# Kernel optimization log

Hardware: AMD Instinct MI355X
Metric: run time of the kernel (lower is better)

The kernel has to match this reference:

```python
import jax, jax.numpy as jnp
import numpy as np

H = 256        # hidden_size
HEADS = 8      # conv1 heads
B = 256        # number of graphs (sessions)
L = 64         # nodes per graph (max_length)
N = B * L      # total nodes
E = 131072     # edges before self-loops
NNODE = 37000  # item vocabulary / num classes


def setup_inputs() -> dict:
    key = jax.random.key(0)
    ks = jax.random.split(key, 16)
    s = 0.02
    return {
        "x_ids": jax.random.randint(ks[0], (N,), 0, NNODE + 1),
        "edge_index": jax.random.randint(ks[1], (2, E), 0, N),
        "batch": jnp.repeat(jnp.arange(B, dtype=jnp.int32), L),
        "emb": jax.random.normal(ks[2], (NNODE + 1, H)) * s,
        "W1": jax.random.normal(ks[3], (H, HEADS * H)) * s,
        "att_src1": jax.random.normal(ks[4], (HEADS, H)) * s,
        "att_dst1": jax.random.normal(ks[5], (HEADS, H)) * s,
        "b1": jnp.zeros((HEADS * H,)),
        "W2": jax.random.normal(ks[6], (HEADS * H, H)) * s,
        "att_src2": jax.random.normal(ks[7], (1, H)) * s,
        "att_dst2": jax.random.normal(ks[8], (1, H)) * s,
        "b2": jnp.zeros((H,)),
        "Wih": jax.random.normal(ks[9], (4 * H, H)) * s,
        "Whh": jax.random.normal(ks[10], (4 * H, H)) * s,
        "bih": jnp.zeros((4 * H,)),
        "bhh": jnp.zeros((4 * H,)),
        "Wp": jax.random.normal(ks[11], (NNODE, H)) * s,
        "bp": jnp.zeros((NNODE,)),
    }


def gat_conv(x, src, dst, W, a_src, a_dst, bias, concat):
    # PyG GATConv: linear -> per-head attention logits -> leaky_relu ->
    # segment-softmax over incoming edges per dst node -> scatter-add.
    n = x.shape[0]
    heads = a_src.shape[0]
    h = (x @ W).reshape(n, heads, -1)                       # [N, heads, out]
    alpha_s = (h * a_src).sum(-1)                            # [N, heads]
    alpha_d = (h * a_dst).sum(-1)
    e = jax.nn.leaky_relu(alpha_s[src] + alpha_d[dst], 0.2)  # [E, heads]
    m = jax.ops.segment_max(e, dst, num_segments=n)
    p = jnp.exp(e - m[dst])
    z = jax.ops.segment_sum(p, dst, num_segments=n)
    alpha = p / (z[dst] + 1e-16)                             # edge softmax
    out = jax.ops.segment_sum(alpha[:, :, None] * h[src], dst, num_segments=n)
    out = out.reshape(n, -1) if concat else out.mean(axis=1)
    return out + bias


def reference(x_ids, edge_index, batch, emb, W1, att_src1, att_dst1, b1,
              W2, att_src2, att_dst2, b2, Wih, Whh, bih, bhh, Wp, bp):
    n = x_ids.shape[0]
    # GATConv default add_self_loops=True
    loops = jnp.arange(n)
    src = jnp.concatenate([edge_index[0], loops])
    dst = jnp.concatenate([edge_index[1], loops])

    emb = emb.at[0].set(0.0)  # padding_idx=0
    x = emb[x_ids]
    # eval mode: dropout is identity
    x = jax.nn.elu(gat_conv(x, src, dst, W1, att_src1, att_dst1, b1, True))
    x = gat_conv(x, src, dst, W2, att_src2, att_dst2, b2, False)  # [N, H]

    # pack variable-length graphs into padded [B, L, H] sequences
    lengths = jax.ops.segment_sum(jnp.ones((n,), jnp.int32), batch, num_segments=B)
    starts = jnp.cumsum(lengths) - lengths
    pos = jnp.arange(n) - starts[batch]
    seq = jnp.zeros((B, L, x.shape[-1]), x.dtype).at[batch, pos].set(x)
    mask = jnp.arange(L)[None, :] < lengths[:, None]  # [B, L]

    # single-layer LSTM; masking emulates pack_padded_sequence: h_n is the
    # hidden state at each sequence's true last timestep
    def step(carry, xs):
        h_prev, c_prev = carry
        x_t, m_t = xs
        g = x_t @ Wih.T + h_prev @ Whh.T + bih + bhh
        i, f, gg, o = jnp.split(g, 4, axis=-1)
        c_new = jax.nn.sigmoid(f) * c_prev + jax.nn.sigmoid(i) * jnp.tanh(gg)
        h_new = jax.nn.sigmoid(o) * jnp.tanh(c_new)
        mm = m_t[:, None]
        return (jnp.where(mm, h_new, h_prev), jnp.where(mm, c_new, c_prev)), None

    h0 = jnp.zeros((B, x.shape[-1]), x.dtype)
    (hT, _), _ = jax.lax.scan(step, (h0, h0),
                              (seq.transpose(1, 0, 2), mask.T))
    return hT @ Wp.T + bp  # [B, NNODE] scores
```

## Files before the change

### kernel.cpp

```cpp
#include <hip/hip_runtime.h>
#include <hip/hip_bf16.h>
#include <cstdint>

#define HD 256
#define NHEADS 8
#define NB 256
#define SL 64
#define NN 16384
#define NE 131072
#define NTOT (NE + NN)

typedef float floatx4 __attribute__((ext_vector_type(4)));
typedef short shortx8 __attribute__((ext_vector_type(8)));
typedef unsigned short ushortx8 __attribute__((ext_vector_type(8)));
typedef unsigned short ushortx4 __attribute__((ext_vector_type(4)));

__device__ __forceinline__ unsigned short f2bf(float f) {
    union { float f; unsigned u; } a; a.f = f;
    unsigned r = a.u + 0x7fffu + ((a.u >> 16) & 1u);
    return (unsigned short)(r >> 16);
}
__device__ __forceinline__ float bf2f(unsigned short b) {
    union { unsigned u; float f; } a; a.u = ((unsigned)b) << 16;
    return a.f;
}

__device__ __forceinline__ void store_b16_sys(unsigned short* p, unsigned v) {
    asm volatile("global_store_short %0, %1, off sc0 sc1" :: "v"(p), "v"(v) : "memory");
}
__device__ __forceinline__ shortx8 load_b128_sys(const unsigned short* p) {
    shortx8 r;
    asm volatile("global_load_dwordx4 %0, %1, off sc0 sc1" : "=v"(r) : "v"(p) : "memory");
    return r;
}


__global__ void k_cast_bf16(const float* __restrict__ in, unsigned short* __restrict__ out, int n4) {
    int i = blockIdx.x * 256 + threadIdx.x;
    if (i >= n4) return;
    float4 v = ((const float4*)in)[i];
    ushortx4 o;
    o[0] = f2bf(v.x); o[1] = f2bf(v.y); o[2] = f2bf(v.z); o[3] = f2bf(v.w);
    *(ushortx4*)&out[i * 4] = o;
}

__global__ void k_transpose_bf16(const float* __restrict__ in, unsigned short* __restrict__ out,
                                 int K, int N) {
    __shared__ float t[32][33];
    int nb = blockIdx.x * 32, kb = blockIdx.y * 32;
    int tx = threadIdx.x, ty = threadIdx.y;
#pragma unroll
    for (int i = 0; i < 4; ++i) {
        int k = kb + ty + i * 8;
        t[ty + i * 8][tx] = in[(size_t)k * N + nb + tx];
    }
    __syncthreads();
#pragma unroll
    for (int i = 0; i < 4; ++i) {
        int nrow = nb + ty + i * 8;
        out[(size_t)nrow * K + kb + tx] = f2bf(t[tx][ty + i * 8]);
    }
}

__global__ void k_add2(const float* __restrict__ a, const float* __restrict__ b,
                       float* __restrict__ o, int n) {
    int i = blockIdx.x * 256 + threadIdx.x;
    if (i < n) o[i] = a[i] + b[i];
}

__global__ void k_zero(int* __restrict__ p, int n) {
    int i = blockIdx.x * 256 + threadIdx.x;
    if (i < n) p[i] = 0;
}

__global__ void k_gather_x(const int* __restrict__ ids, const float* __restrict__ emb,
                           unsigned short* __restrict__ xb) {
    int i = blockIdx.x * 256 + threadIdx.x;
    int n = i >> 6, d4 = (i & 63) << 2;
    int id = ids[n];
    float4 v = make_float4(0.f, 0.f, 0.f, 0.f);
    if (id != 0) v = *(const float4*)&emb[(size_t)id * HD + d4];
    ushortx4 o;
    o[0] = f2bf(v.x); o[1] = f2bf(v.y); o[2] = f2bf(v.z); o[3] = f2bf(v.w);
    *(ushortx4*)&xb[(size_t)n * HD + d4] = o;
}


template <bool OUT_BF16, bool HAS_BIAS>
__global__ __launch_bounds__(256, 2) void k_gemm_bt(
    const unsigned short* __restrict__ A, const unsigned short* __restrict__ B,
    void* __restrict__ C, const float* __restrict__ bias, int M, int Nn, int K) {
    constexpr int LDT = 56;
    __shared__ unsigned short As[128 * LDT];
    __shared__ unsigned short Bs[128 * LDT];
    int tid = threadIdx.x;
    int wave = tid >> 6, lane = tid & 63;
    int q = lane >> 4, c16 = lane & 15;
    long m0 = (long)blockIdx.x * 128;
    long n0 = (long)blockIdx.y * 128;
    int wm = (wave & 1) << 6, wn = (wave >> 1) << 6;
    floatx4 acc[4][4] = {};
    int lrow = tid >> 2;
    int lk = (tid & 3) << 3;
    const unsigned short* Arow0 = A + (m0 + lrow) * K + lk;
    const unsigned short* Arow1 = A + (m0 + 64 + lrow) * K + lk;
    long nb0 = n0 + lrow;      if (nb0 >= Nn) nb0 = Nn - 1;
    long nb1 = n0 + 64 + lrow; if (nb1 >= Nn) nb1 = Nn - 1;
    const unsigned short* Brow0 = B + nb0 * K + lk;
    const unsigned short* Brow1 = B + nb1 * K + lk;

    for (int k0 = 0; k0 < K; k0 += 32) {
        ushortx8 a0 = *(const ushortx8*)(Arow0 + k0);
        ushortx8 a1 = *(const ushortx8*)(Arow1 + k0);
        ushortx8 b0 = *(const ushortx8*)(Brow0 + k0);
        ushortx8 b1 = *(const ushortx8*)(Brow1 + k0);
        __syncthreads();
        *(ushortx8*)&As[lrow * LDT + lk] = a0;
        *(ushortx8*)&As[(64 + lrow) * LDT + lk] = a1;
        *(ushortx8*)&Bs[lrow * LDT + lk] = b0;
        *(ushortx8*)&Bs[(64 + lrow) * LDT + lk] = b1;
        __syncthreads();
        shortx8 af[4], bfr[4];
#pragma unroll
        for (int mt = 0; mt < 4; ++mt)
            af[mt] = *(const shortx8*)&As[(wm + mt * 16 + c16) * LDT + q * 8];
#pragma unroll
        for (int nt = 0; nt < 4; ++nt)
            bfr[nt] = *(const shortx8*)&Bs[(wn + nt * 16 + c16) * LDT + q * 8];
#pragma unroll
        for (int mt = 0; mt < 4; ++mt)
#pragma unroll
            for (int nt = 0; nt < 4; ++nt)
                acc[mt][nt] = __builtin_amdgcn_mfma_f32_16x16x32_bf16(af[mt], bfr[nt], acc[mt][nt], 0, 0, 0);
    }
#pragma unroll
    for (int mt = 0; mt < 4; ++mt) {
        long row_base = m0 + wm + mt * 16 + q * 4;
#pragma unroll
        for (int nt = 0; nt < 4; ++nt) {
            long col = n0 + wn + nt * 16 + c16;
            if (col >= Nn) continue;
            float bv = HAS_BIAS ? bias[col] : 0.0f;
#pragma unroll
            for (int r = 0; r < 4; ++r) {
                float v = acc[mt][nt][r] + bv;
                long idx = (row_base + r) * (long)Nn + col;
                if (OUT_BF16) ((unsigned short*)C)[idx] = f2bf(v);
                else          ((float*)C)[idx] = v;
            }
        }
    }
}

__global__ __launch_bounds__(256, 2) void k_gemm_b8(
    const unsigned short* __restrict__ Ab, const unsigned short* __restrict__ W1t,
    unsigned short* __restrict__ C, const float* __restrict__ b1) {
    constexpr int LDT = 56;
    __shared__ unsigned short As[128 * LDT];
    __shared__ unsigned short Bs[128 * LDT];
    int tid = threadIdx.x;
    int wave = tid >> 6, lane = tid & 63;
    int q = lane >> 4, c16 = lane & 15;
    int hh = blockIdx.z;
    const unsigned short* A = Ab + (size_t)hh * NN * 256;
    const unsigned short* B = W1t + (size_t)hh * 256 * 256;
    long m0 = (long)blockIdx.x * 128;
    long n0 = (long)blockIdx.y * 128;
    int wm = (wave & 1) << 6, wn = (wave >> 1) << 6;
    floatx4 acc[4][4] = {};
    int lrow = tid >> 2;
    int lk = (tid & 3) << 3;
    const unsigned short* Arow0 = A + (m0 + lrow) * 256 + lk;
    const unsigned short* Arow1 = A + (m0 + 64 + lrow) * 256 + lk;
    const unsigned short* Brow0 = B + (n0 + lrow) * 256 + lk;
    const unsigned short* Brow1 = B + (n0 + 64 + lrow) * 256 + lk;

    for (int k0 = 0; k0 < 256; k0 += 32) {
        ushortx8 a0 = *(const ushortx8*)(Arow0 + k0);
        ushortx8 a1 = *(const ushortx8*)(Arow1 + k0);
        ushortx8 b0 = *(const ushortx8*)(Brow0 + k0);
        ushortx8 b1 = *(const ushortx8*)(Brow1 + k0);
        __syncthreads();
        *(ushortx8*)&As[lrow * LDT + lk] = a0;
        *(ushortx8*)&As[(64 + lrow) * LDT + lk] = a1;
        *(ushortx8*)&Bs[lrow * LDT + lk] = b0;
        *(ushortx8*)&Bs[(64 + lrow) * LDT + lk] = b1;
        __syncthreads();
        shortx8 af[4], bfr[4];
#pragma unroll
        for (int mt = 0; mt < 4; ++mt)
            af[mt] = *(const shortx8*)&As[(wm + mt * 16 + c16) * LDT + q * 8];
#pragma unroll
        for (int nt = 0; nt < 4; ++nt)
            bfr[nt] = *(const shortx8*)&Bs[(wn + nt * 16 + c16) * LDT + q * 8];
#pragma unroll
        for (int mt = 0; mt < 4; ++mt)
#pragma unroll
            for (int nt = 0; nt < 4; ++nt)
                acc[mt][nt] = __builtin_amdgcn_mfma_f32_16x16x32_bf16(af[mt], bfr[nt], acc[mt][nt], 0, 0, 0);
    }
#pragma unroll
    for (int mt = 0; mt < 4; ++mt) {
        long row_base = m0 + wm + mt * 16 + q * 4;
#pragma unroll
        for (int nt = 0; nt < 4; ++nt) {
            int gcol = hh * 256 + (int)(n0 + wn + nt * 16 + c16);
            float bv = b1[gcol];
#pragma unroll
            for (int r = 0; r < 4; ++r) {
                float v = acc[mt][nt][r] + bv;
                v = v > 0.f ? v : expm1f(v);
                C[(row_base + r) * 2048 + gcol] = f2bf(v);
            }
        }
    }
}

__global__ void k_build_v(const float* __restrict__ W1, const float* __restrict__ as1,
                          const float* __restrict__ ad1, unsigned short* __restrict__ Vb) {
    __shared__ float av[256];
    int o = blockIdx.x, k = threadIdx.x;
    int hh = o & 7;
    const float* a = (o < 8) ? as1 : ad1;
    av[k] = a[hh * 256 + k];
    __syncthreads();
    const float* wrow = W1 + (size_t)k * 2048 + hh * 256;
    float sum = 0.f;
#pragma unroll 8
    for (int d = 0; d < 256; ++d) sum += wrow[d] * av[d];
    Vb[o * 256 + k] = f2bf(sum);
}


__global__ void k_alpha2(const unsigned short* __restrict__ x2b, const float* __restrict__ asrc,
                         const float* __restrict__ adst, float* __restrict__ als,
                         float* __restrict__ ald) {
    int n = blockIdx.x, t = threadIdx.x;
    ushortx4 hv = *(const ushortx4*)&x2b[(size_t)n * 256 + t * 4];
    float s = 0.f, d = 0.f;
#pragma unroll
    for (int j = 0; j < 4; ++j) {
        float f = bf2f(hv[j]);
        s += f * asrc[t * 4 + j];
        d += f * adst[t * 4 + j];
    }
    for (int o = 32; o; o >>= 1) { s += __shfl_down(s, o, 64); d += __shfl_down(d, o, 64); }
    if (t == 0) { als[n] = s; ald[n] = d; }
}


__global__ void k_deg_init(int* __restrict__ deg) {
    int i = blockIdx.x * 256 + threadIdx.x;
    if (i < NN) deg[i] = 1;
}
__global__ void k_deg_count(const int* __restrict__ ei, int* __restrict__ deg) {
    int e = blockIdx.x * 256 + threadIdx.x;
    if (e < NE) atomicAdd(&deg[ei[NE + e]], 1);
}
__global__ void k_scan(const int* __restrict__ deg, int* __restrict__ row_start,
                       int* __restrict__ cursor) {
    __shared__ int s[1024];
    int t = threadIdx.x;
    int base = t * 16;
    int loc[16]; int sum = 0;
#pragma unroll
    for (int i = 0; i < 16; ++i) { loc[i] = deg[base + i]; sum += loc[i]; }
    s[t] = sum;
    __syncthreads();
    for (int o = 1; o < 1024; o <<= 1) {
        int v = (t >= o) ? s[t - o] : 0;
        __syncthreads();
        s[t] += v;
        __syncthreads();
    }
    int ex = s[t] - sum;
#pragma unroll
    for (int i = 0; i < 16; ++i) {
        row_start[base + i] = ex;
        cursor[base + i] = ex;
        ex += loc[i];
    }
    if (t == 0) row_start[NN] = NTOT;
}
__global__ void k_fill(const int* __restrict__ ei, int* __restrict__ cursor,
                       int* __restrict__ csr_src) {
    int e = blockIdx.x * 256 + threadIdx.x;
    if (e >= NTOT) return;
    int s, d;
    if (e < NE) { s = ei[e]; d = ei[NE + e]; }
    else        { s = e - NE; d = s; }
    int p = atomicAdd(&cursor[d], 1);
    csr_src[p] = s;
}

__global__ __launch_bounds__(256) void k_aggx(
    const int* __restrict__ row_start, const int* __restrict__ csr_src,
    const float* __restrict__ D, const unsigned short* __restrict__ xb,
    unsigned short* __restrict__ aggxb) {
    int n = blockIdx.x, t = threadIdx.x;
    int rs = row_start[n];
    int deg = row_start[n + 1] - rs;
    __shared__ float sad[8], sm[8], sinvz[8];
    __shared__ int sed[32];
    __shared__ float wlds[32][8];
    if (t < 8) sad[t] = D[n * 16 + 8 + t];
    __syncthreads();
    int hh = t >> 5, ii = t & 31;
    float adh = sad[hh];
    float lm = -1e30f;
    for (int i = ii; i < deg; i += 32) {
        int s = csr_src[rs + i];
        float e = D[s * 16 + hh] + adh;
        e = e >= 0.f ? e : 0.2f * e;
        lm = fmaxf(lm, e);
    }
    for (int o = 16; o; o >>= 1) lm = fmaxf(lm, __shfl_down(lm, o, 32));
    if (ii == 0) sm[hh] = lm;
    __syncthreads();
    float mh = sm[hh];
    float lz = 0.f;
    for (int i = ii; i < deg; i += 32) {
        int s = csr_src[rs + i];
        float e = D[s * 16 + hh] + adh;
        e = e >= 0.f ? e : 0.2f * e;
        lz += expf(e - mh);
    }
    for (int o = 16; o; o >>= 1) lz += __shfl_down(lz, o, 32);
    if (ii == 0) sinvz[hh] = 1.0f / (lz + 1e-16f);
    __syncthreads();

    float acc[8] = {0.f, 0.f, 0.f, 0.f, 0.f, 0.f, 0.f, 0.f};
    int eh = t & 7, ee = t >> 3;
    for (int base = 0; base < deg; base += 32) {
        int cnt = min(32, deg - base);
        if (t < 32) sed[t] = (t < cnt) ? csr_src[rs + base + t] : 0;
        __syncthreads();
        if (ee < cnt) {
            int s = sed[ee];
            float e = D[s * 16 + eh] + sad[eh];
            e = e >= 0.f ? e : 0.2f * e;
            wlds[ee][eh] = expf(e - sm[eh]) * sinvz[eh];
        }
        __syncthreads();
        for (int e = 0; e < cnt; ++e) {
            float xv = bf2f(xb[(size_t)sed[e] * 256 + t]);
#pragma unroll
            for (int h = 0; h < 8; ++h) acc[h] += wlds[e][h] * xv;
        }
        __syncthreads();
    }
#pragma unroll
    for (int h = 0; h < 8; ++h)
        aggxb[((size_t)h * NN + n) * 256 + t] = f2bf(acc[h]);
}


__global__ void k_agg2(const int* __restrict__ row_start, const int* __restrict__ csr_src,
                       const float* __restrict__ als, const float* __restrict__ ald,
                       const unsigned short* __restrict__ x2b, const float* __restrict__ b2,
                       unsigned short* __restrict__ out2b) {
    int n = blockIdx.x, t = threadIdx.x;
    int rs = row_start[n];
    int deg = row_start[n + 1] - rs;
    float adn = ald[n];
    float lm = -1e30f;
    for (int i = t; i < deg; i += 64) {
        float e = als[csr_src[rs + i]] + adn;
        e = e >= 0.f ? e : 0.2f * e;
        lm = fmaxf(lm, e);
    }
    for (int o = 32; o; o >>= 1) lm = fmaxf(lm, __shfl_down(lm, o, 64));
    float mh = __shfl(lm, 0, 64);
    float lz = 0.f;
    for (int i = t; i < deg; i += 64) {
        float e = als[csr_src[rs + i]] + adn;
        e = e >= 0.f ? e : 0.2f * e;
        lz += expf(e - mh);
    }
    for (int o = 32; o; o >>= 1) lz += __shfl_down(lz, o, 64);
    float zz = __shfl(lz, 0, 64);
    float inv_z = 1.0f / (zz + 1e-16f);
    float acc[4] = {0.f, 0.f, 0.f, 0.f};
    for (int i = 0; i < deg; ++i) {
        int s = csr_src[rs + i];
        float e = als[s] + adn;
        e = e >= 0.f ? e : 0.2f * e;
        float w = expf(e - mh) * inv_z;
        ushortx4 hv = *(const ushortx4*)&x2b[(size_t)s * 256 + t * 4];
#pragma unroll
        for (int j = 0; j < 4; ++j) acc[j] += w * bf2f(hv[j]);
    }
    ushortx4 o4;
#pragma unroll
    for (int j = 0; j < 4; ++j) o4[j] = f2bf(acc[j] + b2[t * 4 + j]);
    *(ushortx4*)&out2b[(size_t)n * 256 + t * 4] = o4;
}

__global__ void k_repack_whh(const unsigned short* __restrict__ Whhb,
                             unsigned short* __restrict__ WhhR) {
    int i = blockIdx.x * 256 + threadIdx.x;
    int lane = i & 63;
    int fi = i >> 6;
    int f = fi & 3, k0 = (fi >> 2) & 7, w = (fi >> 5) & 3, s = fi >> 7;
    int q = lane >> 4, c16 = lane & 15;
    int gcol = f * 256 + s * 64 + w * 16 + c16;
    int k = k0 * 32 + q * 8;
    ushortx8 v = *(const ushortx8*)&Whhb[(size_t)gcol * 256 + k];
    *(ushortx8*)&WhhR[(size_t)fi * 512 + lane * 8] = v;
}


__global__ __launch_bounds__(256, 1) void k_lstm8(
    const float* __restrict__ Xg, const unsigned short* __restrict__ WhhR,
    unsigned short* __restrict__ hX, int* __restrict__ flags) {
    __shared__ unsigned short wlds[4 * 32 * 512];

    int tid = threadIdx.x;
    int w = tid >> 6, lane = tid & 63;
    int q = lane >> 4, c16 = lane & 15;
    int g = blockIdx.x & 15, s = blockIdx.x >> 4;
    int scol = s * 64 + w * 16 + c16;
    const int fbase = g * 64;

    const unsigned short* wsrc = WhhR + (size_t)((s * 4 + w) * 32) * 512 + lane * 8;
#pragma unroll
    for (int fi = 0; fi < 32; ++fi)
        *(shortx8*)&wlds[(w * 32 + fi) * 512 + lane * 8] =
            *(const shortx8*)(wsrc + fi * 512);

    float cst[4] = {0.f, 0.f, 0.f, 0.f};

    for (int t = 0; t < SL; ++t) {
        float xg[4][4];
#pragma unroll
        for (int r = 0; r < 4; ++r) {
            const float* xp = Xg + ((size_t)(g * 16 + q * 4 + r) * SL + t) * 1024 + scol;
#pragma unroll
            for (int f = 0; f < 4; ++f) xg[r][f] = xp[f * 256];
        }

        floatx4 acc[4] = {};
        if (t > 0) {
            if (tid == 0) {
                int spins = 0;
                while (__hip_atomic_fetch_add(&flags[fbase + t - 1], 0, __ATOMIC_RELAXED,
                                              __HIP_MEMORY_SCOPE_AGENT) < 4) {
                    __builtin_amdgcn_s_sleep(2);
                    if (++spins > 65536) break;
                }
            }
            __syncthreads();

            const unsigned short* hp =
                hX + ((size_t)(t - 1) * 256 + g * 16 + c16) * 256 + q * 8;
            shortx8 af[8];
#pragma unroll
            for (int k0 = 0; k0 < 8; ++k0) af[k0] = load_b128_sys(hp + k0 * 32);
            asm volatile("s_waitcnt vmcnt(0)" ::: "memory");
            __builtin_amdgcn_sched_barrier(0);
#pragma unroll
            for (int k0 = 0; k0 < 8; ++k0)
#pragma unroll
                for (int f = 0; f < 4; ++f) {
                    shortx8 b = *(const shortx8*)&wlds[(w * 32 + k0 * 4 + f) * 512 + lane * 8];
                    acc[f] = __builtin_amdgcn_mfma_f32_16x16x32_bf16(af[k0], b, acc[f], 0, 0, 0);
                }
        }

        unsigned short* hw = hX + ((size_t)t * 256 + g * 16) * 256 + scol;
#pragma unroll
        for (int r = 0; r < 4; ++r) {
            float gi = acc[0][r] + xg[r][0];
            float gf = acc[1][r] + xg[r][1];
            float gG = acc[2][r] + xg[r][2];
            float go = acc[3][r] + xg[r][3];
            float si = __builtin_amdgcn_rcpf(1.f + __expf(-gi));
            float sf = __builtin_amdgcn_rcpf(1.f + __expf(-gf));
            float so = __builtin_amdgcn_rcpf(1.f + __expf(-go));
            float tg = 1.f - 2.f * __builtin_amdgcn_rcpf(1.f + __expf(2.f * gG));
            float c = sf * cst[r] + si * tg;
            cst[r] = c;
            float tc = 1.f - 2.f * __builtin_amdgcn_rcpf(1.f + __expf(2.f * c));
            store_b16_sys(hw + (q * 4 + r) * 256, (unsigned)f2bf(so * tc));
        }

        if (t < SL - 1) {
            asm volatile("s_waitcnt vmcnt(0)" ::: "memory");
            __syncthreads();
            if (tid == 0)
                __hip_atomic_fetch_add(&flags[fbase + t], 1, __ATOMIC_RELAXED,
                                       __HIP_MEMORY_SCOPE_AGENT);
        }
    }
}


extern "C" void kernel_launch(void* const* d_in, const int* in_sizes, int n_in,
                              void* d_out, int out_size, void* d_ws, size_t ws_size,
                              hipStream_t stream) {
    const int*   x_ids = (const int*)d_in[0];
    const int*   ei    = (const int*)d_in[1];
    const float* emb   = (const float*)d_in[3];
    const float* W1    = (const float*)d_in[4];
    const float* as1w  = (const float*)d_in[5];
    const float* ad1w  = (const float*)d_in[6];
    const float* b1    = (const float*)d_in[7];
    const float* W2    = (const float*)d_in[8];
    const float* as2w  = (const float*)d_in[9];
    const float* ad2w  = (const float*)d_in[10];
    const float* b2    = (const float*)d_in[11];
    const float* Wih   = (const float*)d_in[12];
    const float* Whh   = (const float*)d_in[13];
    const float* bih   = (const float*)d_in[14];
    const float* bhh   = (const float*)d_in[15];
    const float* Wp    = (const float*)d_in[16];
    const float* bp    = (const float*)d_in[17];

    char* ws = (char*)d_ws;
    size_t off = 0;
    auto alloc = [&](size_t bytes) -> void* {
        void* p = ws + off;
        off += (bytes + 255) & ~(size_t)255;
        return p;
    };
    unsigned short* U     = (unsigned short*)alloc((size_t)8 * NN * 256 * 2);
    unsigned short* aggxb = U;
    float*          Xg    = (float*)U;
    unsigned short* out1b = (unsigned short*)alloc((size_t)NN * 2048 * 2);
    unsigned short* hX    = out1b;
    unsigned short* xb    = (unsigned short*)alloc((size_t)NN * 256 * 2);
    unsigned short* x2b   = (unsigned short*)alloc((size_t)NN * 256 * 2);
    unsigned short* out2b = (unsigned short*)alloc((size_t)NN * 256 * 2);
    unsigned short* W1t   = (unsigned short*)alloc((size_t)2048 * 256 * 2);
    unsigned short* W2t   = (unsigned short*)alloc((size_t)256 * 2048 * 2);
    unsigned short* Wihb  = (unsigned short*)alloc((size_t)1024 * 256 * 2);
    unsigned short* Whhb  = (unsigned short*)alloc((size_t)1024 * 256 * 2);
    unsigned short* WhhR  = (unsigned short*)alloc((size_t)1024 * 256 * 2);
    unsigned short* Wpb   = (unsigned short*)alloc((size_t)37000 * 256 * 2);
    unsigned short* Vb    = (unsigned short*)alloc((size_t)16 * 256 * 2);
    float*          bb    = (float*)alloc(1024 * 4);
    float*          D     = (float*)alloc((size_t)NN * 16 * 4);
    float*          als2  = (float*)alloc((size_t)NN * 4);
    float*          ald2  = (float*)alloc((size_t)NN * 4);
    unsigned short* hTb   = (unsigned short*)alloc((size_t)256 * 256 * 2);
    int* deg       = (int*)alloc((size_t)NN * 4);
    int* row_start = (int*)alloc((size_t)(NN + 1) * 4);
    int* cursor    = (int*)alloc((size_t)NN * 4);
    int* csr_src   = (int*)alloc((size_t)NTOT * 4);
    int* flags     = (int*)alloc((size_t)16 * 64 * 4);
    (void)ws_size; (void)in_sizes; (void)n_in; (void)out_size; (void)hTb;

    k_transpose_bf16<<<dim3(2048 / 32, 256 / 32), dim3(32, 8), 0, stream>>>(W1, W1t, 256, 2048);
    k_transpose_bf16<<<dim3(256 / 32, 2048 / 32), dim3(32, 8), 0, stream>>>(W2, W2t, 2048, 256);
    k_cast_bf16<<<(262144 / 4 + 255) / 256, 256, 0, stream>>>(Wih, Wihb, 262144 / 4);
    k_cast_bf16<<<(262144 / 4 + 255) / 256, 256, 0, stream>>>(Whh, Whhb, 262144 / 4);
    k_cast_bf16<<<(9472000 / 4 + 255) / 256, 256, 0, stream>>>(Wp, Wpb, 9472000 / 4);
    k_add2<<<4, 256, 0, stream>>>(bih, bhh, bb, 1024);
    k_repack_whh<<<32768 / 256, 256, 0, stream>>>(Whhb, WhhR);
    k_zero<<<4, 256, 0, stream>>>(flags, 1024);
    k_build_v<<<16, 256, 0, stream>>>(W1, as1w, ad1w, Vb);

    k_deg_init<<<NN / 256, 256, 0, stream>>>(deg);
    k_deg_count<<<NE / 256, 256, 0, stream>>>(ei, deg);
    k_scan<<<1, 1024, 0, stream>>>(deg, row_start, cursor);
    k_fill<<<(NTOT + 255) / 256, 256, 0, stream>>>(ei, cursor, csr_src);

    k_gather_x<<<NN * 64 / 256, 256, 0, stream>>>(x_ids, emb, xb);

    k_gemm_bt<false, false><<<dim3(NN / 128, 1), 256, 0, stream>>>(
        xb, Vb, D, nullptr, NN, 16, 256);
    k_aggx<<<NN, 256, 0, stream>>>(row_start, csr_src, D, xb, aggxb);
    k_gemm_b8<<<dim3(NN / 128, 2, 8), 256, 0, stream>>>(aggxb, W1t, out1b, b1);

    k_gemm_bt<true, false><<<dim3(NN / 128, 256 / 128), 256, 0, stream>>>(
        out1b, W2t, x2b, nullptr, NN, 256, 2048);
    k_alpha2<<<NN, 64, 0, stream>>>(x2b, as2w, ad2w, als2, ald2);
    k_agg2<<<NN, 64, 0, stream>>>(row_start, csr_src, als2, ald2, x2b, b2, out2b);

    k_gemm_bt<false, true><<<dim3(NN / 128, 1024 / 128), 256, 0, stream>>>(
        out2b, Wihb, Xg, bb, NN, 1024, 256);
    k_lstm8<<<64, 256, 0, stream>>>(Xg, WhhR, hX, flags);

    k_gemm_bt<false, true><<<dim3(256 / 128, (37000 + 127) / 128), 256, 0, stream>>>(
        hX + (size_t)63 * 256 * 256, Wpb, (float*)d_out, bp, 256, 37000, 256);
}
```

Measured before the change: 618.4 us.

## Stage LSTM hidden outputs in LDS and sync per wave via flags

After: 608.5 us. No clear change (-1.6%).

```diff
diff --git a/kernel.cpp b/kernel.cpp
--- a/kernel.cpp
+++ b/kernel.cpp
@@ -14,6 +14,7 @@
 typedef short shortx8 __attribute__((ext_vector_type(8)));
 typedef unsigned short ushortx8 __attribute__((ext_vector_type(8)));
 typedef unsigned short ushortx4 __attribute__((ext_vector_type(4)));
+typedef unsigned uintx2 __attribute__((ext_vector_type(2)));
 
 __device__ __forceinline__ unsigned short f2bf(float f) {
     union { float f; unsigned u; } a; a.f = f;
@@ -25,12 +26,18 @@
     return a.f;
 }
 
-__device__ __forceinline__ void store_b16_sys(unsigned short* p, unsigned v) {
-    asm volatile("global_store_short %0, %1, off sc0 sc1" :: "v"(p), "v"(v) : "memory");
+__device__ __forceinline__ void store_b64_sys(unsigned short* p, uintx2 v) {
+    asm volatile("global_store_dwordx2 %0, %1, off sc0 sc1" :: "v"(p), "v"(v) : "memory");
 }
 __device__ __forceinline__ shortx8 load_b128_sys(const unsigned short* p) {
     shortx8 r;
     asm volatile("global_load_dwordx4 %0, %1, off sc0 sc1" : "=v"(r) : "v"(p) : "memory");
+    return r;
+}
+__device__ __forceinline__ unsigned load_b32_sys(const int* p) {
+    unsigned r;
+    asm volatile("global_load_dword %0, %1, off sc0 sc1" : "=v"(r) : "v"(p) : "memory");
+    asm volatile("s_waitcnt vmcnt(0)" ::: "memory");
     return r;
 }
 
@@ -410,10 +417,11 @@
 }
 
 
-__global__ __launch_bounds__(256, 1) void k_lstm8(
+__global__ __launch_bounds__(256, 1) void k_lstm10(
     const float* __restrict__ Xg, const unsigned short* __restrict__ WhhR,
     unsigned short* __restrict__ hX, int* __restrict__ flags) {
     __shared__ unsigned short wlds[4 * 32 * 512];
+    __shared__ unsigned short hstage[16 * 68];
 
     int tid = threadIdx.x;
     int w = tid >> 6, lane = tid & 63;
@@ -429,6 +437,7 @@
             *(const shortx8*)(wsrc + fi * 512);
 
     float cst[4] = {0.f, 0.f, 0.f, 0.f};
+    int srow = tid >> 4, scol4 = (tid & 15) * 4;
 
     for (int t = 0; t < SL; ++t) {
         float xg[4][4];
@@ -441,15 +450,10 @@
 
         floatx4 acc[4] = {};
         if (t > 0) {
-            if (tid == 0) {
-                int spins = 0;
-                while (__hip_atomic_fetch_add(&flags[fbase + t - 1], 0, __ATOMIC_RELAXED,
-                                              __HIP_MEMORY_SCOPE_AGENT) < 4) {
-                    __builtin_amdgcn_s_sleep(2);
-                    if (++spins > 65536) break;
-                }
+            int spins = 0;
+            while (load_b32_sys(&flags[fbase + t - 1]) < 16u) {
+                if (++spins > 30000) break;
             }
-            __syncthreads();
 
             const unsigned short* hp =
                 hX + ((size_t)(t - 1) * 256 + g * 16 + c16) * 256 + q * 8;
@@ -467,7 +471,6 @@
                 }
         }
 
-        unsigned short* hw = hX + ((size_t)t * 256 + g * 16) * 256 + scol;
 #pragma unroll
         for (int r = 0; r < 4; ++r) {
             float gi = acc[0][r] + xg[r][0];
@@ -481,16 +484,16 @@
             float c = sf * cst[r] + si * tg;
             cst[r] = c;
             float tc = 1.f - 2.f * __builtin_amdgcn_rcpf(1.f + __expf(2.f * c));
-            store_b16_sys(hw + (q * 4 + r) * 256, (unsigned)f2bf(so * tc));
-        }
-
-        if (t < SL - 1) {
-            asm volatile("s_waitcnt vmcnt(0)" ::: "memory");
-            __syncthreads();
-            if (tid == 0)
-                __hip_atomic_fetch_add(&flags[fbase + t], 1, __ATOMIC_RELAXED,
-                                       __HIP_MEMORY_SCOPE_AGENT);
-        }
+            hstage[(q * 4 + r) * 68 + w * 16 + c16] = f2bf(so * tc);
+        }
+        __syncthreads();
+
+        uintx2 v2 = *(const uintx2*)&hstage[srow * 68 + scol4];
+        store_b64_sys(hX + ((size_t)t * 256 + g * 16 + srow) * 256 + s * 64 + scol4, v2);
+        asm volatile("s_waitcnt vmcnt(0)" ::: "memory");
+        if (t < SL - 1 && lane == 0)
+            __hip_atomic_fetch_add(&flags[fbase + t], 1, __ATOMIC_RELAXED,
+                                   __HIP_MEMORY_SCOPE_AGENT);
     }
 }
 
@@ -542,13 +545,12 @@
     float*          D     = (float*)alloc((size_t)NN * 16 * 4);
     float*          als2  = (float*)alloc((size_t)NN * 4);
     float*          ald2  = (float*)alloc((size_t)NN * 4);
-    unsigned short* hTb   = (unsigned short*)alloc((size_t)256 * 256 * 2);
     int* deg       = (int*)alloc((size_t)NN * 4);
     int* row_start = (int*)alloc((size_t)(NN + 1) * 4);
     int* cursor    = (int*)alloc((size_t)NN * 4);
     int* csr_src   = (int*)alloc((size_t)NTOT * 4);
     int* flags     = (int*)alloc((size_t)16 * 64 * 4);
-    (void)ws_size; (void)in_sizes; (void)n_in; (void)out_size; (void)hTb;
+    (void)ws_size; (void)in_sizes; (void)n_in; (void)out_size;
 
     k_transpose_bf16<<<dim3(2048 / 32, 256 / 32), dim3(32, 8), 0, stream>>>(W1, W1t, 256, 2048);
     k_transpose_bf16<<<dim3(256 / 32, 2048 / 32), dim3(32, 8), 0, stream>>>(W2, W2t, 2048, 256);
@@ -579,7 +581,7 @@
 
     k_gemm_bt<false, true><<<dim3(NN / 128, 1024 / 128), 256, 0, stream>>>(
         out2b, Wihb, Xg, bb, NN, 1024, 256);
-    k_lstm8<<<64, 256, 0, stream>>>(Xg, WhhR, hX, flags);
+    k_lstm10<<<64, 256, 0, stream>>>(Xg, WhhR, hX, flags);
 
     k_gemm_bt<false, true><<<dim3(256 / 128, (37000 + 127) / 128), 256, 0, stream>>>(
         hX + (size_t)63 * 256 * 256, Wpb, (float*)d_out, bp, 256, 37000, 256);
```
